# Kernel tuning notes

Measured on AMD Instinct MI355X. Metric: run time of the kernel, lower is better.

The kernel has to match this reference:

```python
import jax, jax.numpy as jnp
import numpy as np

S, B, C = 7, 2, 20
LC, LN = 5.0, 0.5  # lambda_coord, lambda_noobj
CELL = 1.0 / S


def _iou(b1, b2):
    # center (x, y, w, h) boxes, broadcastable [..., 4]
    x1a, y1a = b1[..., 0] - b1[..., 2] / 2, b1[..., 1] - b1[..., 3] / 2
    x2a, y2a = b1[..., 0] + b1[..., 2] / 2, b1[..., 1] + b1[..., 3] / 2
    x1b, y1b = b2[..., 0] - b2[..., 2] / 2, b2[..., 1] - b2[..., 3] / 2
    x2b, y2b = b2[..., 0] + b2[..., 2] / 2, b2[..., 1] + b2[..., 3] / 2
    iw = jnp.maximum(jnp.minimum(x2a, x2b) - jnp.maximum(x1a, x1b), 0.0)
    ih = jnp.maximum(jnp.minimum(y2a, y2b) - jnp.maximum(y1a, y1b), 0.0)
    inter = iw * ih
    union = b1[..., 2] * b1[..., 3] + b2[..., 2] * b2[..., 3] - inter
    return inter / jnp.maximum(union, 1e-10)


def setup_inputs() -> dict:
    key = jax.random.key(0)
    k1, k2, k3 = jax.random.split(key, 3)
    N, T = 16384, 16
    outputs = jax.random.normal(k1, (N, S, S, B * 5 + C), dtype=jnp.float32)
    # normalized xywh, kept strictly inside (0,1) so grid indices are valid
    boxes = jax.random.uniform(k2, (N, T, 4), dtype=jnp.float32, minval=0.01, maxval=0.99)
    labels = jax.random.randint(k3, (N, T), 1, C + 1)  # class labels in 1..C
    return {"outputs": outputs, "boxes": boxes, "labels": labels}


def reference(outputs, boxes, labels):
    N = outputs.shape[0]
    T = boxes.shape[1]
    bbox = outputs[..., : B * 5].reshape(N, S, S, B, 5)
    conf = bbox[..., 4]                         # [N,S,S,B]
    cls_logits = outputs[..., B * 5:]           # [N,S,S,C]
    # decode predicted centers to absolute image coords (as in the original)
    gx = jnp.arange(S, dtype=outputs.dtype)[None, :, None]  # column index
    gy = jnp.arange(S, dtype=outputs.dtype)[:, None, None]  # row index
    px = (bbox[..., 0] + gx) * CELL
    py = (bbox[..., 1] + gy) * CELL
    pred = jnp.stack([px, py, bbox[..., 2], bbox[..., 3]], axis=-1)  # [N,S,S,B,4]

    tx, ty, tw, th = boxes[..., 0], boxes[..., 1], boxes[..., 2], boxes[..., 3]  # [N,T]
    gxi = (tx * S).astype(jnp.int32)
    gyi = (ty * S).astype(jnp.int32)
    offx = tx * S - gxi.astype(tx.dtype)
    offy = ty * S - gyi.astype(ty.dtype)

    bi = jnp.arange(N)[:, None]  # [N,1] broadcasts with [N,T]
    cell_pred = pred[bi, gyi, gxi]          # [N,T,B,4]
    cell_conf = conf[bi, gyi, gxi]          # [N,T,B]
    cell_cls = cls_logits[bi, gyi, gxi]     # [N,T,C]

    ious = _iou(boxes[:, :, None, :], cell_pred)   # [N,T,B]
    best = (B - 1) - jnp.argmax(ious[..., ::-1], axis=-1)  # [N,T]

    bp = jnp.take_along_axis(cell_pred, best[:, :, None, None], axis=2)[:, :, 0, :]  # [N,T,4]
    bconf = jnp.take_along_axis(cell_conf, best[:, :, None], axis=2)[:, :, 0]        # [N,T]

    eps = 1e-6
    box_loss = (
        (bp[..., 0] - offx) ** 2
        + (bp[..., 1] - offy) ** 2
        + (jnp.sqrt(jnp.maximum(bp[..., 2], eps)) - jnp.sqrt(jnp.maximum(tw, eps))) ** 2
        + (jnp.sqrt(jnp.maximum(bp[..., 3], eps)) - jnp.sqrt(jnp.maximum(th, eps))) ** 2
    ).sum(axis=-1)                                     # [N]
    obj_loss = ((bconf - 1.0) ** 2).sum(axis=-1)        # [N]

    probs = jax.nn.softmax(cell_cls, axis=-1)           # [N,T,C]
    onehot = jax.nn.one_hot(labels - 1, C, dtype=probs.dtype)
    class_loss = ((probs - onehot) ** 2).sum(axis=-1).sum(axis=-1)  # [N]

    obj_mask = jnp.zeros((N, S, S, B), dtype=bool).at[bi, gyi, gxi, best].set(True)
    nm = ~obj_mask
    cnt = nm.sum(axis=(1, 2, 3)).astype(conf.dtype)     # always > 0 (T < S*S*B)
    noobj_loss = (conf ** 2 * nm).sum(axis=(1, 2, 3)) / cnt  # mean over unmasked conf

    per_img = LC * box_loss + class_loss + obj_loss + LN * noobj_loss
    return per_img.mean()
```

## Files before the change

kernel.cpp:

```cpp
#include <hip/hip_runtime.h>

#define Cnum 20
#define NCH  30
#define NCONF 98
#define IMGF 1470
#define IPB  4
#define LCf 5.0f
#define LNf 0.5f

__global__ __launch_bounds__(256) void yolo_loss_kernel(
    const float* __restrict__ outputs,
    const float* __restrict__ boxes,
    const int*   __restrict__ labels,
    float*       __restrict__ per_img)
{
    const int tid  = threadIdx.x;
    const int wave = tid >> 6;
    const int lane = tid & 63;
    const int n0   = blockIdx.x * IPB;
    const int n    = n0 + wave;
    const int t    = lane >> 2;
    const int q    = lane & 3;

    __shared__ float s_all[IPB * IMGF];

    const float* gsrc = outputs + (size_t)n0 * IMGF;
    #pragma unroll
    for (int k = 0; k < 6; ++k) {
        int j = tid + k * 256;
        if (j < (IPB * IMGF) / 4) {
            __builtin_amdgcn_global_load_lds(
                (const __attribute__((address_space(1))) void*)(gsrc + (size_t)j * 4),
                (__attribute__((address_space(3))) void*)((char*)s_all + (size_t)(k * 256 + wave * 64) * 16),
                16, 0, 0);
        }
    }

    const float4 bx = reinterpret_cast<const float4*>(boxes)[(size_t)n * 16 + t];
    const int   lab = labels[(size_t)n * 16 + t] - 1;

    __syncthreads();

    const float* img = s_all + wave * IMGF;

    const float tx = bx.x, ty = bx.y, tw = bx.z, th = bx.w;
    const float fx = tx * 7.0f, fy = ty * 7.0f;
    const int gxi = (int)fx, gyi = (int)fy;
    const float offx = fx - (float)gxi;
    const float offy = fy - (float)gyi;
    const int cellIdx = gyi * 7 + gxi;
    const float* cell = img + cellIdx * NCH;

    float ns;
    {
        int c = lane >> 1, b = lane & 1;
        float cf = img[c * NCH + b * 5 + 4];
        ns = cf * cf;
        if (lane < NCONF - 64) {
            int s2 = lane + 64;
            int c2 = s2 >> 1, b2 = s2 & 1;
            float cf2 = img[c2 * NCH + b2 * 5 + 4];
            ns += cf2 * cf2;
        }
    }

    float px = 0.f, py = 0.f, pw = 0.f, ph = 0.f, pc = 0.f, iou_own = 0.f;
    if (q < 2) {
        float rx = cell[q * 5 + 0];
        float ry = cell[q * 5 + 1];
        pw       = cell[q * 5 + 2];
        ph       = cell[q * 5 + 3];
        pc       = cell[q * 5 + 4];
        px = (rx + (float)gxi) * (1.0f / 7.0f);
        py = (ry + (float)gyi) * (1.0f / 7.0f);

        float x1a = tx - tw * 0.5f, y1a = ty - th * 0.5f;
        float x2a = tx + tw * 0.5f, y2a = ty + th * 0.5f;
        float x1b = px - pw * 0.5f, y1b = py - ph * 0.5f;
        float x2b = px + pw * 0.5f, y2b = py + ph * 0.5f;
        float iw = fmaxf(fminf(x2a, x2b) - fmaxf(x1a, x1b), 0.0f);
        float ih = fmaxf(fminf(y2a, y2b) - fmaxf(y1a, y1b), 0.0f);
        float inter = iw * ih;
        float uni = tw * th + pw * ph - inter;
        iou_own = inter / fmaxf(uni, 1e-10f);
    }
    const float iou_other = __shfl_xor(iou_own, 1);
    int bestq = 0;
    if (q < 2) {
        float i0 = (q == 0) ? iou_own   : iou_other;
        float i1 = (q == 0) ? iou_other : iou_own;
        bestq = (i1 >= i0) ? 1 : 0;
    }
    const int best = __shfl(bestq, lane & ~3);
    const int s = cellIdx * 2 + best;

    float contrib = 0.0f;
    const float eps = 1e-6f;
    if (q == best) {
        float dx = px - offx, dy = py - offy;
        float dw = sqrtf(fmaxf(pw, eps)) - sqrtf(fmaxf(tw, eps));
        float dh = sqrtf(fmaxf(ph, eps)) - sqrtf(fmaxf(th, eps));
        float box_l = dx * dx + dy * dy + dw * dw + dh * dh;
        float obj_l = (pc - 1.0f) * (pc - 1.0f);
        contrib = LCf * box_l + obj_l;
    }

    bool firstv = true;
    #pragma unroll
    for (int j = 0; j < 15; ++j) {
        int sj = __shfl(s, 4 * j);
        if (j < t && sj == s) firstv = false;
    }
    float ms = 0.0f, mc = 0.0f;
    if (q == best && firstv) { ms = pc * pc; mc = 1.0f; }

    {
        float cv[5];
        #pragma unroll
        for (int i = 0; i < 5; ++i) cv[i] = cell[10 + q * 5 + i];
        float m = fmaxf(fmaxf(fmaxf(cv[0], cv[1]), fmaxf(cv[2], cv[3])), cv[4]);
        m = fmaxf(m, __shfl_xor(m, 1));
        m = fmaxf(m, __shfl_xor(m, 2));
        float esum = 0.f, e2 = 0.f, elab = 0.f;
        #pragma unroll
        for (int i = 0; i < 5; ++i) {
            float e = __expf(cv[i] - m);
            esum += e; e2 += e * e;
            if (q * 5 + i == lab) elab = e;
        }
        esum += __shfl_xor(esum, 1);  esum += __shfl_xor(esum, 2);
        e2   += __shfl_xor(e2,   1);  e2   += __shfl_xor(e2,   2);
        elab += __shfl_xor(elab, 1);  elab += __shfl_xor(elab, 2);
        if (q == 0) {
            float inv = 1.0f / esum;
            contrib += e2 * inv * inv - 2.0f * elab * inv + 1.0f;
        }
    }

    #pragma unroll
    for (int off = 32; off > 0; off >>= 1) {
        contrib += __shfl_xor(contrib, off);
        ms      += __shfl_xor(ms,      off);
        mc      += __shfl_xor(mc,      off);
        ns      += __shfl_xor(ns,      off);
    }
    if (lane == 0)
        per_img[n] = contrib + LNf * (ns - ms) / (98.0f - mc);
}

__global__ __launch_bounds__(1024) void reduce_mean_kernel(
    const float* __restrict__ per_img, float* __restrict__ out, int N)
{
    __shared__ double sd[16];
    double acc = 0.0;
    const float4* p4 = reinterpret_cast<const float4*>(per_img);
    for (int i = threadIdx.x; i < N / 4; i += 1024) {
        float4 v = p4[i];
        acc += (double)v.x + (double)v.y + (double)v.z + (double)v.w;
    }
    #pragma unroll
    for (int off = 32; off > 0; off >>= 1) acc += __shfl_xor(acc, off);
    if ((threadIdx.x & 63) == 0) sd[threadIdx.x >> 6] = acc;
    __syncthreads();
    if (threadIdx.x == 0) {
        double t = 0.0;
        #pragma unroll
        for (int w = 0; w < 16; ++w) t += sd[w];
        out[0] = (float)(t / (double)N);
    }
}

extern "C" void kernel_launch(void* const* d_in, const int* in_sizes, int n_in,
                              void* d_out, int out_size, void* d_ws, size_t ws_size,
                              hipStream_t stream) {
    const float* outputs = (const float*)d_in[0];
    const float* boxes   = (const float*)d_in[1];
    const int*   labels  = (const int*)d_in[2];
    float* out = (float*)d_out;

    const int N = in_sizes[0] / IMGF;
    float* per_img = (float*)d_ws;

    yolo_loss_kernel<<<N / IPB, 256, 0, stream>>>(outputs, boxes, labels, per_img);
    reduce_mean_kernel<<<1, 1024, 0, stream>>>(per_img, out, N);
}
```

Measured before the change: 25.84 us.

## Process two images per wave with wave-local LDS loads and LDS-based dedup

Each wave now handles two images, loading its own pair of images into LDS and waiting only on its own loads (vmcnt) instead of a block-wide barrier. The O(T) shuffle loop that detects duplicate object cells is replaced by an LDS scatter-and-check plus a ballot and popcount. Per-image results are summed per wave, so the final reduction reads half as many partials with a smaller block. This doubles LDS per block to about 47KB, which lowers occupancy, and relies on LDS write-then-read ordering within a single wave for the dedup.

Measured after the change: 26.69 us. 3.3% more time.

```diff
diff --git a/kernel.cpp b/kernel.cpp
--- a/kernel.cpp
+++ b/kernel.cpp
@@ -1,56 +1,21 @@
 #include <hip/hip_runtime.h>
 
-#define Cnum 20
-#define NCH  30
+#define NCH   30
 #define NCONF 98
-#define IMGF 1470
-#define IPB  4
+#define IMGF  1470
+#define IPB   8
+#define PAIR4 735
 #define LCf 5.0f
 #define LNf 0.5f
 
-__global__ __launch_bounds__(256) void yolo_loss_kernel(
-    const float* __restrict__ outputs,
-    const float* __restrict__ boxes,
-    const int*   __restrict__ labels,
-    float*       __restrict__ per_img)
+#define AS1 __attribute__((address_space(1)))
+#define AS3 __attribute__((address_space(3)))
+
+__device__ __forceinline__ float img_partial(const float* __restrict__ img,
+                                             float4 bx, int lab,
+                                             volatile unsigned char* sm,
+                                             int lane, int t, int q)
 {
-    const int tid  = threadIdx.x;
-    const int wave = tid >> 6;
-    const int lane = tid & 63;
-    const int n0   = blockIdx.x * IPB;
-    const int n    = n0 + wave;
-    const int t    = lane >> 2;
-    const int q    = lane & 3;
-
-    __shared__ float s_all[IPB * IMGF];
-
-    const float* gsrc = outputs + (size_t)n0 * IMGF;
-    #pragma unroll
-    for (int k = 0; k < 6; ++k) {
-        int j = tid + k * 256;
-        if (j < (IPB * IMGF) / 4) {
-            __builtin_amdgcn_global_load_lds(
-                (const __attribute__((address_space(1))) void*)(gsrc + (size_t)j * 4),
-                (__attribute__((address_space(3))) void*)((char*)s_all + (size_t)(k * 256 + wave * 64) * 16),
-                16, 0, 0);
-        }
-    }
-
-    const float4 bx = reinterpret_cast<const float4*>(boxes)[(size_t)n * 16 + t];
-    const int   lab = labels[(size_t)n * 16 + t] - 1;
-
-    __syncthreads();
-
-    const float* img = s_all + wave * IMGF;
-
-    const float tx = bx.x, ty = bx.y, tw = bx.z, th = bx.w;
-    const float fx = tx * 7.0f, fy = ty * 7.0f;
-    const int gxi = (int)fx, gyi = (int)fy;
-    const float offx = fx - (float)gxi;
-    const float offy = fy - (float)gyi;
-    const int cellIdx = gyi * 7 + gxi;
-    const float* cell = img + cellIdx * NCH;
-
     float ns;
     {
         int c = lane >> 1, b = lane & 1;
@@ -64,6 +29,14 @@
         }
     }
 
+    const float tx = bx.x, ty = bx.y, tw = bx.z, th = bx.w;
+    const float fx = tx * 7.0f, fy = ty * 7.0f;
+    const int gxi = (int)fx, gyi = (int)fy;
+    const float offx = fx - (float)gxi;
+    const float offy = fy - (float)gyi;
+    const int cellIdx = gyi * 7 + gxi;
+    const float* cell = img + cellIdx * NCH;
+
     float px = 0.f, py = 0.f, pw = 0.f, ph = 0.f, pc = 0.f, iou_own = 0.f;
     if (q < 2) {
         float rx = cell[q * 5 + 0];
@@ -105,14 +78,13 @@
         contrib = LCf * box_l + obj_l;
     }
 
-    bool firstv = true;
-    #pragma unroll
-    for (int j = 0; j < 15; ++j) {
-        int sj = __shfl(s, 4 * j);
-        if (j < t && sj == s) firstv = false;
-    }
-    float ms = 0.0f, mc = 0.0f;
-    if (q == best && firstv) { ms = pc * pc; mc = 1.0f; }
+    if (q == best) sm[s] = (unsigned char)lane;
+    asm volatile("s_waitcnt lgkmcnt(0)" ::: "memory");
+    __builtin_amdgcn_sched_barrier(0);
+    const bool winner = (q == best) && (sm[s] == (unsigned char)lane);
+    const unsigned long long bal = __ballot(winner);
+    const int mc = __popcll(bal);
+    const float ms = winner ? pc * pc : 0.0f;
 
     {
         float cv[5];
@@ -137,24 +109,68 @@
         }
     }
 
+    const float invDen = 1.0f / (98.0f - (float)mc);
+    return contrib + LNf * (ns - ms) * invDen;
+}
+
+__global__ __launch_bounds__(256) void yolo_loss_kernel(
+    const float* __restrict__ outputs,
+    const float* __restrict__ boxes,
+    const int*   __restrict__ labels,
+    float*       __restrict__ pair_sum)
+{
+    const int tid  = threadIdx.x;
+    const int wave = tid >> 6;
+    const int lane = tid & 63;
+    const int t    = lane >> 2;
+    const int q    = lane & 3;
+    const int n0   = blockIdx.x * IPB + wave * 2;
+
+    __shared__ float         s_buf[IPB * IMGF];
+    __shared__ unsigned char s_m[4][2][112];
+
+    const float4* out4 = reinterpret_cast<const float4*>(outputs);
+    const size_t pbase = (size_t)(n0 >> 1) * PAIR4;
+    char* wbase = (char*)s_buf + (size_t)wave * (PAIR4 * 16);
     #pragma unroll
-    for (int off = 32; off > 0; off >>= 1) {
-        contrib += __shfl_xor(contrib, off);
-        ms      += __shfl_xor(ms,      off);
-        mc      += __shfl_xor(mc,      off);
-        ns      += __shfl_xor(ns,      off);
-    }
-    if (lane == 0)
-        per_img[n] = contrib + LNf * (ns - ms) / (98.0f - mc);
-}
-
-__global__ __launch_bounds__(1024) void reduce_mean_kernel(
-    const float* __restrict__ per_img, float* __restrict__ out, int N)
+    for (int k = 0; k < 11; ++k) {
+        __builtin_amdgcn_global_load_lds(
+            (const AS1 void*)(out4 + pbase + k * 64 + lane),
+            (AS3 void*)(wbase + (size_t)k * 64 * 16), 16, 0, 0);
+    }
+    if (lane < PAIR4 - 704) {
+        __builtin_amdgcn_global_load_lds(
+            (const AS1 void*)(out4 + pbase + 704 + lane),
+            (AS3 void*)(wbase + (size_t)704 * 16), 16, 0, 0);
+    }
+
+    const float4* bx4 = reinterpret_cast<const float4*>(boxes);
+    const float4 bx0 = bx4[(size_t)n0 * 16 + t];
+    const float4 bx1 = bx4[(size_t)(n0 + 1) * 16 + t];
+    const int   lab0 = labels[(size_t)n0 * 16 + t] - 1;
+    const int   lab1 = labels[(size_t)(n0 + 1) * 16 + t] - 1;
+
+    asm volatile("s_waitcnt vmcnt(0)" ::: "memory");
+    __builtin_amdgcn_sched_barrier(0);
+
+    const float* img0 = s_buf + (size_t)wave * 2 * IMGF;
+    const float* img1 = img0 + IMGF;
+
+    float v = img_partial(img0, bx0, lab0, s_m[wave][0], lane, t, q)
+            + img_partial(img1, bx1, lab1, s_m[wave][1], lane, t, q);
+
+    #pragma unroll
+    for (int off = 32; off > 0; off >>= 1) v += __shfl_xor(v, off);
+    if (lane == 0) pair_sum[blockIdx.x * 4 + wave] = v;
+}
+
+__global__ __launch_bounds__(256) void reduce_mean_kernel(
+    const float* __restrict__ pair_sum, float* __restrict__ out, int np, int N)
 {
-    __shared__ double sd[16];
+    __shared__ double sd[4];
     double acc = 0.0;
-    const float4* p4 = reinterpret_cast<const float4*>(per_img);
-    for (int i = threadIdx.x; i < N / 4; i += 1024) {
+    const float4* p4 = reinterpret_cast<const float4*>(pair_sum);
+    for (int i = threadIdx.x; i < np / 4; i += 256) {
         float4 v = p4[i];
         acc += (double)v.x + (double)v.y + (double)v.z + (double)v.w;
     }
@@ -162,12 +178,8 @@
     for (int off = 32; off > 0; off >>= 1) acc += __shfl_xor(acc, off);
     if ((threadIdx.x & 63) == 0) sd[threadIdx.x >> 6] = acc;
     __syncthreads();
-    if (threadIdx.x == 0) {
-        double t = 0.0;
-        #pragma unroll
-        for (int w = 0; w < 16; ++w) t += sd[w];
-        out[0] = (float)(t / (double)N);
-    }
+    if (threadIdx.x == 0)
+        out[0] = (float)(((sd[0] + sd[1]) + (sd[2] + sd[3])) / (double)N);
 }
 
 extern "C" void kernel_launch(void* const* d_in, const int* in_sizes, int n_in,
@@ -178,9 +190,11 @@
     const int*   labels  = (const int*)d_in[2];
     float* out = (float*)d_out;
 
-    const int N = in_sizes[0] / IMGF;
-    float* per_img = (float*)d_ws;
-
-    yolo_loss_kernel<<<N / IPB, 256, 0, stream>>>(outputs, boxes, labels, per_img);
-    reduce_mean_kernel<<<1, 1024, 0, stream>>>(per_img, out, N);
-}
+    const int N  = in_sizes[0] / IMGF;
+    const int nb = N / IPB;
+    const int np = nb * 4;
+    float* pair_sum = (float*)d_ws;
+
+    yolo_loss_kernel<<<nb, 256, 0, stream>>>(outputs, boxes, labels, pair_sum);
+    reduce_mean_kernel<<<1, 256, 0, stream>>>(pair_sum, out, np, N);
+}
```
